# Kernel tuning notes

Hardware: AMD Instinct MI355X
Metric: run time of the kernel (lower is better)

Reference implementation:

```python
import jax, jax.numpy as jnp
import numpy as np

L = 16            # clip_len
STRIDES = (2, 2)
RADII = (0.15, 0.3)
NSAMPLES = (16, 32)
EPS = 1e-5
NEG_SLOPE = 0.2


def _fps(xyz, npoint):
    # furthest point sampling, xyz: (N, 3) -> (npoint,) int32 indices, start at 0
    N = xyz.shape[0]
    def step(carry, _):
        mind, last = carry
        d = jnp.sum((xyz - xyz[last]) ** 2, axis=-1)
        mind = jnp.minimum(mind, d)
        nxt = jnp.argmax(mind).astype(jnp.int32)
        return (mind, nxt), nxt
    _, rest = jax.lax.scan(step, (jnp.full((N,), 1e10, xyz.dtype), jnp.int32(0)), None, length=npoint - 1)
    return jnp.concatenate([jnp.zeros((1,), jnp.int32), rest])


def _shift_point(xyz, batch, N):
    # torch.roll(points, -1, dims=1) over the temporal axis, with last-frame extrapolation fix
    p = xyz.reshape(batch // L, L, N, 3)
    s = jnp.roll(p, -1, axis=1)
    shift_mean = jnp.mean(s[:, :-1] - p[:, :-1], axis=1)   # (Bc, N, 3)
    s = s.at[:, -1].set(p[:, -1] + shift_mean)
    return s.reshape(batch, N, 3)


def _conv_bn_lrelu(x, w, g, b):
    # 1x1 Conv2d (no bias) + GroupBN (per-channel over all other dims) + LeakyReLU(0.2)
    y = jnp.einsum('oc,bcnk->bonk', w, x)
    mu = jnp.mean(y, axis=(0, 2, 3), keepdims=True)
    var = jnp.var(y, axis=(0, 2, 3), keepdims=True)
    y = (y - mu) * jax.lax.rsqrt(var + EPS) * g[None, :, None, None] + b[None, :, None, None]
    return jnp.where(y > 0, y, NEG_SLOPE * y)


def _sa_module(xyz, features, stride, radius, nsample, layers):
    # xyz: (B, N, 3), features: (B, C, N)
    batch, N = xyz.shape[0], xyz.shape[1]
    q = _shift_point(xyz, batch, N)
    npoint = N // stride if stride > 1 else N
    if stride > 1:
        idx = jax.vmap(lambda p: _fps(p, npoint))(jax.lax.stop_gradient(q))  # (B, npoint)
        q = jax.vmap(lambda p, ix: p[ix])(q, idx)                            # (B, npoint, 3)
    # ball query: first `nsample` neighbors of each query within `radius`, padded with first hit
    d2 = jnp.sum((q[:, :, None, :] - xyz[:, None, :, :]) ** 2, axis=-1)      # (B, npoint, N)
    mask = d2 < radius * radius
    cand = jnp.where(mask, jnp.arange(N, dtype=jnp.int32)[None, None, :], N)
    srt = jnp.sort(cand, axis=-1)[..., :nsample]
    first = srt[..., :1]
    gidx = jnp.where(srt == N, first, srt)
    gidx = jnp.where(gidx == N, 0, gidx)                                     # fallback: no neighbor
    grouped_xyz = jax.vmap(lambda pts, ix: pts[ix])(xyz, gidx)               # (B, npoint, ns, 3)
    dp = (grouped_xyz - q[:, :, None, :]) / radius                           # normalize_dp
    dist = jnp.linalg.norm(dp, axis=-1)                                      # (B, npoint, ns) -> 4th grouped channel
    feats = jnp.swapaxes(features, 1, 2)                                     # (B, N, C)
    grouped_f = jax.vmap(lambda f, ix: f[ix])(feats, gidx)                   # (B, npoint, ns, C)
    x = jnp.concatenate([dp, grouped_f], axis=-1)                            # (B, npoint, ns, 3 + C)
    x = jnp.transpose(x, (0, 3, 1, 2))                                       # (B, 3 + C, npoint, ns)
    for (w, g, b) in layers:
        x = _conv_bn_lrelu(x, w, g, b)
    gate = jax.nn.sigmoid(dist)[:, None, :, :]                               # sigmoid(points[:, -1:])
    out = jnp.max(gate * x, axis=-1)                                         # (B, Cout, npoint)
    return q, out


def _forward(xyz, w1a, g1a, b1a, w1b, g1b, b1b, w2a, g2a, b2a, w2b, g2b, b2b):
    features = jnp.swapaxes(xyz, 1, 2)                                       # features default = xyz^T
    q1, f1 = _sa_module(xyz, features, STRIDES[0], RADII[0], NSAMPLES[0],
                        [(w1a, g1a, b1a), (w1b, g1b, b1b)])
    q2, f2 = _sa_module(q1, f1, STRIDES[1], RADII[1], NSAMPLES[1],
                        [(w2a, g2a, b2a), (w2b, g2b, b2b)])
    return f2                                                                # (32, 256, 128)


def setup_inputs() -> dict:
    key = jax.random.key(0)
    ks = jax.random.split(key, 5)
    B, N = 32, 512   # B = 2 clips * clip_len 16
    xyz = jax.random.uniform(ks[0], (B, N, 3), jnp.float32)
    def w(k, o, i):
        return jax.random.normal(k, (o, i), jnp.float32) / np.sqrt(i).astype(np.float32)
    return {
        'xyz': xyz,
        'w1a': w(ks[1], 64, 6),    'g1a': jnp.ones(64),  'b1a': jnp.zeros(64),
        'w1b': w(ks[2], 128, 64),  'g1b': jnp.ones(128), 'b1b': jnp.zeros(128),
        'w2a': w(ks[3], 128, 131), 'g2a': jnp.ones(128), 'b2a': jnp.zeros(128),
        'w2b': w(ks[4], 256, 128), 'g2b': jnp.ones(256), 'b2b': jnp.zeros(256),
    }


def reference(xyz, w1a, g1a, b1a, w1b, g1b, b1b, w2a, g2a, b2a, w2b, g2b, b2b):
    return _forward(xyz, w1a, g1a, b1a, w1b, g1b, b1b, w2a, g2a, b2a, w2b, g2b, b2b)
```

## Files before the change

kernel.cpp:

```cpp
#include <hip/hip_runtime.h>
#include <hip/hip_bf16.h>
#include <math.h>


#define BATCH 32
#define MCOLS 131072
#define CGRID 2048

typedef __attribute__((ext_vector_type(8))) short short8;
typedef __attribute__((ext_vector_type(4))) short short4v;
typedef __attribute__((ext_vector_type(4))) float f32x4;

__device__ __forceinline__ float b2f(short s) {
    return __uint_as_float(((unsigned)(unsigned short)s) << 16);
}
__device__ __forceinline__ short f2b(float f) {
    __hip_bfloat16 h = __float2bfloat16(f);
    return (short)__builtin_bit_cast(unsigned short, h);
}
__device__ __forceinline__ float dpp_row16_sum(float v) {
    int x;
    x = __builtin_amdgcn_update_dpp(0, __float_as_int(v), 0x111, 0xf, 0xf, true);
    v += __int_as_float(x);
    x = __builtin_amdgcn_update_dpp(0, __float_as_int(v), 0x112, 0xf, 0xf, true);
    v += __int_as_float(x);
    x = __builtin_amdgcn_update_dpp(0, __float_as_int(v), 0x114, 0xf, 0xf, true);
    v += __int_as_float(x);
    x = __builtin_amdgcn_update_dpp(0, __float_as_int(v), 0x118, 0xf, 0xf, true);
    v += __int_as_float(x);
    return v;
}
template<int C>
__device__ __forceinline__ float dpp_max(float v) {
    int x = __builtin_amdgcn_update_dpp(0, __float_as_int(v), C, 0xf, 0xf, true);
    return fmaxf(v, __int_as_float(x));
}
__device__ __forceinline__ float readlane_f(float v, int lane) {
    return __int_as_float(__builtin_amdgcn_readlane(__float_as_int(v), lane));
}

__device__ __forceinline__ void prep_elem(const float* __restrict__ w, int O, int C,
                                          int CK, short* __restrict__ hi,
                                          short* __restrict__ lo, int t) {
    if (t >= O * CK) return;
    int o = t / CK, c = t % CK;
    float f = (c < C) ? w[o * C + c] : 0.f;
    short h = f2b(f);
    float fh = b2f(h);
    int NT = O >> 4;
    int ot = o >> 4, l15 = o & 15;
    int kc = c >> 5, quad = (c & 31) >> 3, j = c & 7;
    size_t idx = (((size_t)kc * NT + ot) * 64 + quad * 16 + l15) * 8 + j;
    hi[idx] = h;
    lo[idx] = f2b(f - fh);
}

__device__ __forceinline__ void shift_elem(const float* __restrict__ xyz,
                                           float* __restrict__ qout, int t, int N) {
    int c = t % 3;
    int n = (t / 3) % N;
    int b = t / (3 * N);
    int l = b & 15;
    float v;
    if (l < 15) {
        v = xyz[((size_t)(b + 1) * N + n) * 3 + c];
    } else {
        int g0 = b - 15;
        float acc = 0.f;
        for (int i = 0; i < 15; ++i) {
            float d = __fsub_rn(xyz[((size_t)(g0 + i + 1) * N + n) * 3 + c],
                                xyz[((size_t)(g0 + i) * N + n) * 3 + c]);
            acc = __fadd_rn(acc, d);
        }
        v = __fadd_rn(xyz[((size_t)b * N + n) * 3 + c], __fdiv_rn(acc, 15.f));
    }
    qout[t] = v;
}

__global__ __launch_bounds__(256) void setup_kernel(
        const float* __restrict__ w1a, const float* __restrict__ w1b,
        const float* __restrict__ w2a, const float* __restrict__ w2b,
        const float* __restrict__ xyz, float* __restrict__ qs1,
        short* w1aH, short* w1aL, short* w1bH, short* w1bL,
        short* w2aH, short* w2aL, short* w2bH, short* w2bL) {
    int bid = blockIdx.x;
    int tid = threadIdx.x;
    if (bid < 8)        prep_elem(w1a, 64, 6, 32,    w1aH, w1aL, bid * 256 + tid);
    else if (bid < 40)  prep_elem(w1b, 128, 64, 64,  w1bH, w1bL, (bid - 8) * 256 + tid);
    else if (bid < 120) prep_elem(w2a, 128, 131, 160, w2aH, w2aL, (bid - 40) * 256 + tid);
    else if (bid < 248) prep_elem(w2b, 256, 128, 128, w2bH, w2bL, (bid - 120) * 256 + tid);
    else {
        int t = (bid - 248) * 256 + tid;
        if (t < BATCH * 512 * 3) shift_elem(xyz, qs1, t, 512);
    }
}

template<int N, int NPOINT>
__global__ __launch_bounds__(64) void fps_kernel(const float* __restrict__ q,
                                                 float* __restrict__ qsel) {
    int b = blockIdx.x;
    int lane = threadIdx.x;
    constexpr int P = N / 64;
    __shared__ float4 qp[N];
    __shared__ int sel[NPOINT];
    const float* qb = q + (size_t)b * N * 3;
    for (int j = lane; j < N; j += 64)
        qp[j] = make_float4(qb[j * 3 + 0], qb[j * 3 + 1], qb[j * 3 + 2], 0.f);
    if (lane == 0) sel[0] = 0;
    __syncthreads();
    float px[P], py[P], pz[P], mind[P];
#pragma unroll
    for (int p = 0; p < P; ++p) {
        float4 v = qp[lane * P + p];
        px[p] = v.x; py[p] = v.y; pz[p] = v.z;
        mind[p] = 1e10f;
    }
    float4 L0 = qp[0];
    float lx = L0.x, ly = L0.y, lz = L0.z;
    for (int s = 1; s < NPOINT; ++s) {
        float mn[P];
#pragma unroll
        for (int p = 0; p < P; ++p) {
            float dx = __fsub_rn(px[p], lx);
            float dy = __fsub_rn(py[p], ly);
            float dz = __fsub_rn(pz[p], lz);
            float d = __fadd_rn(__fadd_rn(__fmul_rn(dx, dx), __fmul_rn(dy, dy)),
                                __fmul_rn(dz, dz));
            float m2 = fminf(mind[p], d);
            mind[p] = m2;
            mn[p] = m2;
        }
        float t[P];
#pragma unroll
        for (int p = 0; p < P; ++p) t[p] = mn[p];
#pragma unroll
        for (int w = P / 2; w >= 1; w >>= 1)
#pragma unroll
            for (int p = 0; p < w; ++p) t[p] = fmaxf(t[p], t[p + w]);
        float local = t[0];
        float m = local;
        m = dpp_max<0x111>(m);
        m = dpp_max<0x112>(m);
        m = dpp_max<0x114>(m);
        m = dpp_max<0x118>(m);
        m = dpp_max<0x142>(m);
        m = dpp_max<0x143>(m);
        float maxd = readlane_f(m, 63);
        int enc = P - 1;
        float bx = px[P - 1], by = py[P - 1], bz = pz[P - 1];
#pragma unroll
        for (int p = P - 2; p >= 0; --p) {
            bool e = (mn[p] == local);
            enc = e ? p : enc;
            bx = e ? px[p] : bx;
            by = e ? py[p] : by;
            bz = e ? pz[p] : bz;
        }
        unsigned long long msk = __ballot(local == maxd);
        int winner = (int)__builtin_ctzll(msk);
        int last = winner * P + __builtin_amdgcn_readlane(enc, winner);
        lx = readlane_f(bx, winner);
        ly = readlane_f(by, winner);
        lz = readlane_f(bz, winner);
        if (lane == 0) sel[s] = last;
    }
    __syncthreads();
    for (int i = lane; i < NPOINT; i += 64) {
        float4 Pt = qp[sel[i]];
        size_t o = ((size_t)b * NPOINT + i) * 3;
        qsel[o + 0] = Pt.x;
        qsel[o + 1] = Pt.y;
        qsel[o + 2] = Pt.z;
    }
}

template<int N, int NPOINT, int NS, int CF, int CK>
__global__ __launch_bounds__(256) void ballq_kernel(
        const float* __restrict__ xyz,
        const float* __restrict__ qpts,
        const float* __restrict__ feats,
        float r2, float radius,
        short* __restrict__ X, float* __restrict__ gate) {
    static_assert((NS & (NS - 1)) == 0, "NS pow2");
    static_assert(CK % 8 == 0, "CK mult of 8");
    int lane = threadIdx.x & 63;
    int wib = threadIdx.x >> 6;
    int wid = blockIdx.x * 4 + wib;
    int b = wid / NPOINT;
    int i = wid % NPOINT;
    const float* qp = qpts + ((size_t)b * NPOINT + i) * 3;
    float qx = qp[0], qy = qp[1], qz = qp[2];
    __shared__ int gsh[4][NS];
    int* gidx = gsh[wib];
    int taken = 0, first = 0;
    bool any = false;
#pragma unroll
    for (int base = 0; base < N; base += 64) {
        int j = base + lane;
        const float* p = xyz + ((size_t)b * N + j) * 3;
        float dx = __fsub_rn(qx, p[0]);
        float dy = __fsub_rn(qy, p[1]);
        float dz = __fsub_rn(qz, p[2]);
        float d2 = __fadd_rn(__fadd_rn(__fmul_rn(dx, dx), __fmul_rn(dy, dy)),
                             __fmul_rn(dz, dz));
        bool in = d2 < r2;
        unsigned long long mk = __ballot(in);
        if (!any && mk) { first = base + __builtin_ctzll(mk); any = true; }
        int cb = __builtin_popcountll(mk & ((1ull << lane) - 1ull));
        int slot = taken + cb;
        if (in && slot < NS) gidx[slot] = j;
        taken += (int)__builtin_popcountll(mk);
    }
    if (taken < NS) {
        for (int s = taken + lane; s < NS; s += 64) gidx[s] = any ? first : 0;
    }
    __syncthreads();
    int m0 = (b * NPOINT + i) * NS;
    if (lane < NS) {
        int g = gidx[lane];
        const float* p = xyz + ((size_t)b * N + g) * 3;
        float dx = (p[0] - qx) / radius;
        float dy = (p[1] - qy) / radius;
        float dz = (p[2] - qz) / radius;
        float dist = sqrtf(dx * dx + dy * dy + dz * dz);
        gate[m0 + lane] = 1.f / (1.f + expf(-dist));
    }
    for (int e8 = lane * 8; e8 < NS * CK; e8 += 64 * 8) {
        int s = e8 / CK;
        int c0 = e8 % CK;
        int g = gidx[s];
        const float* frow = feats + (size_t)(b * N + g) * CF;
        const float* prow = xyz + ((size_t)b * N + g) * 3;
        short8 v8;
#pragma unroll
        for (int ii = 0; ii < 8; ++ii) {
            int c = c0 + ii;
            float v;
            if (c < 3) {
                float qc = (c == 0) ? qx : ((c == 1) ? qy : qz);
                v = (prow[c] - qc) / radius;
            } else if (c < 3 + CF) {
                v = frow[c - 3];
            } else {
                v = 0.f;
            }
            v8[ii] = f2b(v);
        }
        *(short8*)(X + (size_t)(m0 + s) * CK + c0) = v8;
    }
}

template<int CK, int O, bool AFF>
__global__ __launch_bounds__(256, 3) void mfma_conv(
        const short* __restrict__ X, const short* __restrict__ Whi,
        const short* __restrict__ Wlo, const float* __restrict__ ss,
        short* __restrict__ Y, float* __restrict__ pS, float* __restrict__ pS2) {
    constexpr int KC = CK / 32;
    constexpr int NT = O / 16;
    constexpr int OW = NT / 4;
    constexpr int LR = CK + 8;
    constexpr int CB = CK / 8;
    __shared__ __align__(16) short xs[64 * LR];
    __shared__ __align__(16) short wh[NT * 512];
    __shared__ __align__(16) short wl[NT * 512];
    __shared__ float ssl[AFF ? 2 * CK : 2];
    __shared__ float sblk[O], s2blk[O];
    int tid = threadIdx.x;
    int m0 = blockIdx.x * 64;

    if constexpr (AFF) {
        for (int i = tid; i < 2 * CK; i += 256) ssl[i] = ss[i];
        __syncthreads();
    }
    for (int idx = tid; idx < 64 * CB; idx += 256) {
        int r = idx / CB;
        int col = (idx % CB) * 8;
        short8 v = *(const short8*)(X + (size_t)(m0 + r) * CK + col);
        if constexpr (AFF) {
#pragma unroll
            for (int i = 0; i < 8; ++i) {
                float f = b2f(v[i]);
                f = fmaf(f, ssl[col + i], ssl[CK + col + i]);
                f = f > 0.f ? f : 0.2f * f;
                v[i] = f2b(f);
            }
        }
        *(short8*)(xs + r * LR + col) = v;
    }

    int lane = tid & 63;
    int wave = tid >> 6;
    int l15 = lane & 15;
    int quad = lane >> 4;
    int obase = wave * OW * 16;

    f32x4 acc[4][OW];
#pragma unroll
    for (int mt = 0; mt < 4; ++mt)
#pragma unroll
        for (int ot = 0; ot < OW; ++ot) acc[mt][ot] = (f32x4){0.f, 0.f, 0.f, 0.f};

    for (int kc = 0; kc < KC; ++kc) {
        __syncthreads();
        {
            const short8* gH = (const short8*)Whi + (size_t)kc * NT * 64;
            const short8* gL = (const short8*)Wlo + (size_t)kc * NT * 64;
            short8* lH = (short8*)wh;
            short8* lL = (short8*)wl;
            for (int i = tid; i < NT * 64; i += 256) { lH[i] = gH[i]; lL[i] = gL[i]; }
        }
        __syncthreads();
        short8 bf[4];
#pragma unroll
        for (int mt = 0; mt < 4; ++mt)
            bf[mt] = *(const short8*)(xs + (mt * 16 + l15) * LR + kc * 32 + quad * 8);
#pragma unroll
        for (int ot = 0; ot < OW; ++ot) {
            short8 ah = ((const short8*)wh)[(wave * OW + ot) * 64 + lane];
            short8 al = ((const short8*)wl)[(wave * OW + ot) * 64 + lane];
#pragma unroll
            for (int mt = 0; mt < 4; ++mt) {
                acc[mt][ot] = __builtin_amdgcn_mfma_f32_16x16x32_bf16(ah, bf[mt], acc[mt][ot], 0, 0, 0);
                acc[mt][ot] = __builtin_amdgcn_mfma_f32_16x16x32_bf16(al, bf[mt], acc[mt][ot], 0, 0, 0);
            }
        }
    }

#pragma unroll
    for (int mt = 0; mt < 4; ++mt) {
        size_t ybase = (size_t)(m0 + mt * 16 + l15) * O + obase + quad * 4;
#pragma unroll
        for (int ot = 0; ot < OW; ++ot) {
            short4v pk;
#pragma unroll
            for (int r4 = 0; r4 < 4; ++r4) pk[r4] = f2b(acc[mt][ot][r4]);
            *(short4v*)(Y + ybase + ot * 16) = pk;
        }
    }
#pragma unroll
    for (int ot = 0; ot < OW; ++ot) {
#pragma unroll
        for (int r4 = 0; r4 < 4; ++r4) {
            float s = 0.f, s2 = 0.f;
#pragma unroll
            for (int mt = 0; mt < 4; ++mt) {
                float v = acc[mt][ot][r4];
                s += v;
                s2 = fmaf(v, v, s2);
            }
            s = dpp_row16_sum(s);
            s2 = dpp_row16_sum(s2);
            if (l15 == 15) {
                int o = obase + ot * 16 + quad * 4 + r4;
                sblk[o] = s;
                s2blk[o] = s2;
            }
        }
    }
    __syncthreads();
    for (int o = tid; o < O; o += 256) {
        pS [(size_t)o * CGRID + blockIdx.x] = sblk[o];
        pS2[(size_t)o * CGRID + blockIdx.x] = s2blk[o];
    }
}

template<int O>
__global__ __launch_bounds__(256) void stats_fin(
        const float* __restrict__ pS, const float* __restrict__ pS2,
        const float* __restrict__ gm, const float* __restrict__ bt,
        float* __restrict__ norm) {
    int o = blockIdx.x;
    float s = 0.f, s2 = 0.f;
    for (int p = threadIdx.x; p < CGRID; p += 256) {
        s += pS[(size_t)o * CGRID + p];
        s2 += pS2[(size_t)o * CGRID + p];
    }
#pragma unroll
    for (int off = 32; off >= 1; off >>= 1) {
        s  += __shfl_xor(s,  off, 64);
        s2 += __shfl_xor(s2, off, 64);
    }
    __shared__ float sh[8];
    int wid = threadIdx.x >> 6;
    if ((threadIdx.x & 63) == 0) { sh[wid] = s; sh[4 + wid] = s2; }
    __syncthreads();
    if (threadIdx.x == 0) {
        float S  = sh[0] + sh[1] + sh[2] + sh[3];
        float S2 = sh[4] + sh[5] + sh[6] + sh[7];
        const float invM = 1.f / (float)MCOLS;
        float mu = S * invM;
        float var = S2 * invM - mu * mu;
        float sc = gm[o] * rsqrtf(var + 1e-5f);
        norm[o] = sc;
        norm[O + o] = bt[o] - mu * sc;
    }
}

__global__ __launch_bounds__(256) void pool1_shift2_kernel(
        const short* __restrict__ Y, const float* __restrict__ norm,
        const float* __restrict__ gate, float* __restrict__ out,
        const float* __restrict__ q1c, float* __restrict__ qs2) {
    constexpr int NS = 16, NPOINT = 256, O = 128;
    if (blockIdx.x >= 4096) {
        int t = (int)(blockIdx.x - 4096) * 256 + threadIdx.x;
        if (t < BATCH * 256 * 3) shift_elem(q1c, qs2, t, 256);
        return;
    }
    int t = blockIdx.x * 256 + threadIdx.x;
    int o = t % O;
    int n = (t / O) % NPOINT;
    int b = t / (O * NPOINT);
    int m0 = (b * NPOINT + n) * NS;
    float sc = norm[o], sf = norm[O + o];
    float best = -INFINITY;
#pragma unroll
    for (int k = 0; k < NS; ++k) {
        float v = fmaf(b2f(Y[(size_t)(m0 + k) * O + o]), sc, sf);
        v = v > 0.f ? v : 0.2f * v;
        best = fmaxf(best, gate[m0 + k] * v);
    }
    out[t] = best;
}

__global__ __launch_bounds__(256) void pool2_kernel(
        const short* __restrict__ Y, const float* __restrict__ norm,
        const float* __restrict__ gate, float* __restrict__ out) {
    constexpr int NS = 32, NPOINT = 128, O = 256;
    int b  = blockIdx.x >> 3;
    int oc = (blockIdx.x >> 1) & 3;
    int nc = blockIdx.x & 1;
    __shared__ float trans[64][65];
    int tid = threadIdx.x;
    for (int w = 0; w < 16; ++w) {
        int idx = w * 256 + tid;
        int o_l = idx & 63;
        int n_l = idx >> 6;
        int o = oc * 64 + o_l;
        int n = nc * 64 + n_l;
        int m0 = (b * NPOINT + n) * NS;
        float sc = norm[o], sf = norm[O + o];
        float best = -INFINITY;
#pragma unroll
        for (int k = 0; k < NS; ++k) {
            float v = fmaf(b2f(Y[(size_t)(m0 + k) * O + o]), sc, sf);
            v = v > 0.f ? v : 0.2f * v;
            best = fmaxf(best, gate[m0 + k] * v);
        }
        trans[o_l][n_l] = best;
    }
    __syncthreads();
    for (int w = 0; w < 16; ++w) {
        int idx = w * 256 + tid;
        int o_l = idx >> 6;
        int n_l = idx & 63;
        out[((size_t)b * O + oc * 64 + o_l) * NPOINT + nc * 64 + n_l] = trans[o_l][n_l];
    }
}

extern "C" void kernel_launch(void* const* d_in, const int* in_sizes, int n_in,
                              void* d_out, int out_size, void* d_ws, size_t ws_size,
                              hipStream_t stream) {
    const float* xyz = (const float*)d_in[0];
    const float* w1a = (const float*)d_in[1];
    const float* g1a = (const float*)d_in[2];
    const float* b1a = (const float*)d_in[3];
    const float* w1b = (const float*)d_in[4];
    const float* g1b = (const float*)d_in[5];
    const float* b1b = (const float*)d_in[6];
    const float* w2a = (const float*)d_in[7];
    const float* g2a = (const float*)d_in[8];
    const float* b2a = (const float*)d_in[9];
    const float* w2b = (const float*)d_in[10];
    const float* g2b = (const float*)d_in[11];
    const float* b2b = (const float*)d_in[12];

    char* ws = (char*)d_ws;
    constexpr size_t OFF_Q1C   = 0;
    constexpr size_t OFF_GATE1 = 98304;
    constexpr size_t OFF_Q2C   = 622592;
    constexpr size_t OFF_GATE2 = 671744;
    constexpr size_t OFF_NORM  = 1196032;
    constexpr size_t OFF_W     = 1204224;
    constexpr size_t OFF_PS    = 1499136;
    constexpr size_t OFF_PS2   = 3596288;
    constexpr size_t OFF_A     = 5693440;
    constexpr size_t OFF_B     = 39247872;
    constexpr size_t OFF_F1    = OFF_B + 41943040;

    float* q1c   = (float*)(ws + OFF_Q1C);
    float* gate1 = (float*)(ws + OFF_GATE1);
    float* q2c   = (float*)(ws + OFF_Q2C);
    float* gate2 = (float*)(ws + OFF_GATE2);
    float* n1a   = (float*)(ws + OFF_NORM);
    float* n1b   = (float*)(ws + OFF_NORM + 512);
    float* n2a   = (float*)(ws + OFF_NORM + 1536);
    float* n2b   = (float*)(ws + OFF_NORM + 2560);
    short* w1aH  = (short*)(ws + OFF_W);
    short* w1aL  = w1aH + 2048;
    short* w1bH  = w1aL + 2048;
    short* w1bL  = w1bH + 8192;
    short* w2aH  = w1bL + 8192;
    short* w2aL  = w2aH + 20480;
    short* w2bH  = w2aL + 20480;
    short* w2bL  = w2bH + 32768;
    float* pS    = (float*)(ws + OFF_PS);
    float* pS2   = (float*)(ws + OFF_PS2);
    float* qs2   = (float*)(ws + OFF_PS);

    char* A = ws + OFF_A;
    char* B = ws + OFF_B;
    short* X1  = (short*)A;
    short* Y1a = (short*)B;
    short* Y1b = (short*)A;
    short* X2  = (short*)B;
    short* Y2a = (short*)A;
    short* Y2b = (short*)B;
    float* qs1 = (float*)B;
    float* f1  = (float*)(ws + OFF_F1);

    const float r2_1 = (float)(0.15 * 0.15);
    const float r2_2 = (float)(0.3 * 0.3);

    setup_kernel<<<440, 256, 0, stream>>>(w1a, w1b, w2a, w2b, xyz, qs1,
                                          w1aH, w1aL, w1bH, w1bL,
                                          w2aH, w2aL, w2bH, w2bL);

    fps_kernel<512, 256><<<32, 64, 0, stream>>>(qs1, q1c);
    ballq_kernel<512, 256, 16, 3, 32><<<2048, 256, 0, stream>>>(
        xyz, q1c, xyz, r2_1, 0.15f, X1, gate1);
    mfma_conv<32, 64, false><<<CGRID, 256, 0, stream>>>(X1, w1aH, w1aL, nullptr, Y1a, pS, pS2);
    stats_fin<64><<<64, 256, 0, stream>>>(pS, pS2, g1a, b1a, n1a);
    mfma_conv<64, 128, true><<<CGRID, 256, 0, stream>>>(Y1a, w1bH, w1bL, n1a, Y1b, pS, pS2);
    stats_fin<128><<<128, 256, 0, stream>>>(pS, pS2, g1b, b1b, n1b);
    pool1_shift2_kernel<<<4192, 256, 0, stream>>>(Y1b, n1b, gate1, f1, q1c, qs2);

    fps_kernel<256, 128><<<32, 64, 0, stream>>>(qs2, q2c);
    ballq_kernel<256, 128, 32, 128, 160><<<1024, 256, 0, stream>>>(
        q1c, q2c, f1, r2_2, 0.3f, X2, gate2);
    mfma_conv<160, 128, false><<<CGRID, 256, 0, stream>>>(X2, w2aH, w2aL, nullptr, Y2a, pS, pS2);
    stats_fin<128><<<128, 256, 0, stream>>>(pS, pS2, g2a, b2a, n2a);
    mfma_conv<128, 256, true><<<CGRID, 256, 0, stream>>>(Y2a, w2bH, w2bL, n2a, Y2b, pS, pS2);
    stats_fin<256><<<256, 256, 0, stream>>>(pS, pS2, g2b, b2b, n2b);
    pool2_kernel<<<256, 256, 0, stream>>>(Y2b, n2b, gate2, (float*)d_out);
}
```

Baseline: 389.6 us.

## Overlap second-stage FPS with first-layer conv by fusing into extra blocks

The stage-2 point shift moves earlier, into the stats kernel after the first conv, and gets its own workspace buffer. The stage-2 furthest point sampling then runs as 32 extra blocks appended to the second conv launch of stage 1, reusing that kernel's shared memory. The goal is to hide the serial, latency-bound FPS behind the MFMA conv work and remove one launch. The cost is that the FPS blocks carry the conv kernel's 256-thread, high-LDS footprint with only 64 threads active. They may also be scheduled last and end up on the critical path.

```diff
diff --git a/kernel.cpp b/kernel.cpp
--- a/kernel.cpp
+++ b/kernel.cpp
@@ -96,18 +96,9 @@
 }
 
 template<int N, int NPOINT>
-__global__ __launch_bounds__(64) void fps_kernel(const float* __restrict__ q,
-                                                 float* __restrict__ qsel) {
-    int b = blockIdx.x;
-    int lane = threadIdx.x;
+__device__ __forceinline__ void fps_spine(const float4* __restrict__ qp,
+                                          int* __restrict__ sel, int lane) {
     constexpr int P = N / 64;
-    __shared__ float4 qp[N];
-    __shared__ int sel[NPOINT];
-    const float* qb = q + (size_t)b * N * 3;
-    for (int j = lane; j < N; j += 64)
-        qp[j] = make_float4(qb[j * 3 + 0], qb[j * 3 + 1], qb[j * 3 + 2], 0.f);
-    if (lane == 0) sel[0] = 0;
-    __syncthreads();
     float px[P], py[P], pz[P], mind[P];
 #pragma unroll
     for (int p = 0; p < P; ++p) {
@@ -164,8 +155,45 @@
         lz = readlane_f(bz, winner);
         if (lane == 0) sel[s] = last;
     }
+}
+
+template<int N, int NPOINT>
+__global__ __launch_bounds__(64) void fps_kernel(const float* __restrict__ q,
+                                                 float* __restrict__ qsel) {
+    int b = blockIdx.x;
+    int lane = threadIdx.x;
+    __shared__ float4 qp[N];
+    __shared__ int sel[NPOINT];
+    const float* qb = q + (size_t)b * N * 3;
+    for (int j = lane; j < N; j += 64)
+        qp[j] = make_float4(qb[j * 3 + 0], qb[j * 3 + 1], qb[j * 3 + 2], 0.f);
+    if (lane == 0) sel[0] = 0;
+    __syncthreads();
+    fps_spine<N, NPOINT>(qp, sel, lane);
     __syncthreads();
     for (int i = lane; i < NPOINT; i += 64) {
+        float4 Pt = qp[sel[i]];
+        size_t o = ((size_t)b * NPOINT + i) * 3;
+        qsel[o + 0] = Pt.x;
+        qsel[o + 1] = Pt.y;
+        qsel[o + 2] = Pt.z;
+    }
+}
+
+__device__ void fps256_body(const float* __restrict__ q, float* __restrict__ qsel,
+                            int b, char* smem) {
+    constexpr int N = 256, NPOINT = 128;
+    float4* qp = (float4*)smem;
+    int* sel = (int*)(smem + N * 16);
+    int tid = threadIdx.x;
+    const float* qb = q + (size_t)b * N * 3;
+    for (int j = tid; j < N; j += 256)
+        qp[j] = make_float4(qb[j * 3 + 0], qb[j * 3 + 1], qb[j * 3 + 2], 0.f);
+    if (tid == 0) sel[0] = 0;
+    __syncthreads();
+    if (tid < 64) fps_spine<N, NPOINT>(qp, sel, tid);
+    __syncthreads();
+    for (int i = tid; i < NPOINT; i += 256) {
         float4 Pt = qp[sel[i]];
         size_t o = ((size_t)b * NPOINT + i) * 3;
         qsel[o + 0] = Pt.x;
@@ -250,11 +278,12 @@
     }
 }
 
-template<int CK, int O, bool AFF>
+template<int CK, int O, bool AFF, bool FUSE>
 __global__ __launch_bounds__(256, 3) void mfma_conv(
         const short* __restrict__ X, const short* __restrict__ Whi,
         const short* __restrict__ Wlo, const float* __restrict__ ss,
-        short* __restrict__ Y, float* __restrict__ pS, float* __restrict__ pS2) {
+        short* __restrict__ Y, float* __restrict__ pS, float* __restrict__ pS2,
+        const float* __restrict__ qs2, float* __restrict__ q2c) {
     constexpr int KC = CK / 32;
     constexpr int NT = O / 16;
     constexpr int OW = NT / 4;
@@ -265,6 +294,13 @@
     __shared__ __align__(16) short wl[NT * 512];
     __shared__ float ssl[AFF ? 2 * CK : 2];
     __shared__ float sblk[O], s2blk[O];
+    static_assert(!FUSE || 64 * LR * 2 >= 256 * 16 + 128 * 4, "fps LDS fits in xs");
+    if constexpr (FUSE) {
+        if (blockIdx.x >= CGRID) {
+            fps256_body(qs2, q2c, (int)blockIdx.x - CGRID, (char*)xs);
+            return;
+        }
+    }
     int tid = threadIdx.x;
     int m0 = blockIdx.x * 64;
 
@@ -396,16 +432,48 @@
     }
 }
 
-__global__ __launch_bounds__(256) void pool1_shift2_kernel(
-        const short* __restrict__ Y, const float* __restrict__ norm,
-        const float* __restrict__ gate, float* __restrict__ out,
+__global__ __launch_bounds__(256) void stats_fin64_shift2(
+        const float* __restrict__ pS, const float* __restrict__ pS2,
+        const float* __restrict__ gm, const float* __restrict__ bt,
+        float* __restrict__ norm,
         const float* __restrict__ q1c, float* __restrict__ qs2) {
-    constexpr int NS = 16, NPOINT = 256, O = 128;
-    if (blockIdx.x >= 4096) {
-        int t = (int)(blockIdx.x - 4096) * 256 + threadIdx.x;
+    constexpr int O = 64;
+    if (blockIdx.x >= O) {
+        int t = (int)(blockIdx.x - O) * 256 + threadIdx.x;
         if (t < BATCH * 256 * 3) shift_elem(q1c, qs2, t, 256);
         return;
     }
+    int o = blockIdx.x;
+    float s = 0.f, s2 = 0.f;
+    for (int p = threadIdx.x; p < CGRID; p += 256) {
+        s += pS[(size_t)o * CGRID + p];
+        s2 += pS2[(size_t)o * CGRID + p];
+    }
+#pragma unroll
+    for (int off = 32; off >= 1; off >>= 1) {
+        s  += __shfl_xor(s,  off, 64);
+        s2 += __shfl_xor(s2, off, 64);
+    }
+    __shared__ float sh[8];
+    int wid = threadIdx.x >> 6;
+    if ((threadIdx.x & 63) == 0) { sh[wid] = s; sh[4 + wid] = s2; }
+    __syncthreads();
+    if (threadIdx.x == 0) {
+        float S  = sh[0] + sh[1] + sh[2] + sh[3];
+        float S2 = sh[4] + sh[5] + sh[6] + sh[7];
+        const float invM = 1.f / (float)MCOLS;
+        float mu = S * invM;
+        float var = S2 * invM - mu * mu;
+        float sc = gm[o] * rsqrtf(var + 1e-5f);
+        norm[o] = sc;
+        norm[O + o] = bt[o] - mu * sc;
+    }
+}
+
+template<int NS, int NPOINT, int O>
+__global__ __launch_bounds__(256) void pool1_kernel(
+        const short* __restrict__ Y, const float* __restrict__ norm,
+        const float* __restrict__ gate, float* __restrict__ out) {
     int t = blockIdx.x * 256 + threadIdx.x;
     int o = t % O;
     int n = (t / O) % NPOINT;
@@ -486,6 +554,7 @@
     constexpr size_t OFF_A     = 5693440;
     constexpr size_t OFF_B     = 39247872;
     constexpr size_t OFF_F1    = OFF_B + 41943040;
+    constexpr size_t OFF_QS2   = 106356736;
 
     float* q1c   = (float*)(ws + OFF_Q1C);
     float* gate1 = (float*)(ws + OFF_GATE1);
@@ -505,7 +574,7 @@
     short* w2bL  = w2bH + 32768;
     float* pS    = (float*)(ws + OFF_PS);
     float* pS2   = (float*)(ws + OFF_PS2);
-    float* qs2   = (float*)(ws + OFF_PS);
+    float* qs2   = (float*)(ws + OFF_QS2);
 
     char* A = ws + OFF_A;
     char* B = ws + OFF_B;
@@ -528,18 +597,21 @@
     fps_kernel<512, 256><<<32, 64, 0, stream>>>(qs1, q1c);
     ballq_kernel<512, 256, 16, 3, 32><<<2048, 256, 0, stream>>>(
         xyz, q1c, xyz, r2_1, 0.15f, X1, gate1);
-    mfma_conv<32, 64, false><<<CGRID, 256, 0, stream>>>(X1, w1aH, w1aL, nullptr, Y1a, pS, pS2);
-    stats_fin<64><<<64, 256, 0, stream>>>(pS, pS2, g1a, b1a, n1a);
-    mfma_conv<64, 128, true><<<CGRID, 256, 0, stream>>>(Y1a, w1bH, w1bL, n1a, Y1b, pS, pS2);
+    mfma_conv<32, 64, false, false><<<CGRID, 256, 0, stream>>>(
+        X1, w1aH, w1aL, nullptr, Y1a, pS, pS2, nullptr, nullptr);
+    stats_fin64_shift2<<<160, 256, 0, stream>>>(pS, pS2, g1a, b1a, n1a, q1c, qs2);
+    mfma_conv<64, 128, true, true><<<CGRID + 32, 256, 0, stream>>>(
+        Y1a, w1bH, w1bL, n1a, Y1b, pS, pS2, qs2, q2c);
     stats_fin<128><<<128, 256, 0, stream>>>(pS, pS2, g1b, b1b, n1b);
-    pool1_shift2_kernel<<<4192, 256, 0, stream>>>(Y1b, n1b, gate1, f1, q1c, qs2);
-
-    fps_kernel<256, 128><<<32, 64, 0, stream>>>(qs2, q2c);
+    pool1_kernel<16, 256, 128><<<4096, 256, 0, stream>>>(Y1b, n1b, gate1, f1);
+
     ballq_kernel<256, 128, 32, 128, 160><<<1024, 256, 0, stream>>>(
         q1c, q2c, f1, r2_2, 0.3f, X2, gate2);
-    mfma_conv<160, 128, false><<<CGRID, 256, 0, stream>>>(X2, w2aH, w2aL, nullptr, Y2a, pS, pS2);
+    mfma_conv<160, 128, false, false><<<CGRID, 256, 0, stream>>>(
+        X2, w2aH, w2aL, nullptr, Y2a, pS, pS2, nullptr, nullptr);
     stats_fin<128><<<128, 256, 0, stream>>>(pS, pS2, g2a, b2a, n2a);
-    mfma_conv<128, 256, true><<<CGRID, 256, 0, stream>>>(Y2a, w2bH, w2bL, n2a, Y2b, pS, pS2);
+    mfma_conv<128, 256, true, false><<<CGRID, 256, 0, stream>>>(
+        Y2a, w2bH, w2bL, n2a, Y2b, pS, pS2, nullptr, nullptr);
     stats_fin<256><<<256, 256, 0, stream>>>(pS, pS2, g2b, b2b, n2b);
     pool2_kernel<<<256, 256, 0, stream>>>(Y2b, n2b, gate2, (float*)d_out);
 }
```

Result: faster. 381.7 us (-2.0%).
